# Kernel tuning notes

Hardware: AMD Instinct MI355X
Metric: run time of the kernel (lower is better)

Reference implementation:

```python
import jax, jax.numpy as jnp
import numpy as np


def setup_inputs() -> dict:
    key = jax.random.key(0)
    k1, k2, k3, k4 = jax.random.split(key, 4)
    B, H, W, K = 16, 256, 256, 313
    pred_ab = jax.random.normal(k1, (B, 2, H, W), dtype=jnp.float32)
    # targets in normalized ab range roughly [-1, 1]
    target_ab = jax.random.uniform(k2, (B, 2, H, W), dtype=jnp.float32, minval=-1.0, maxval=1.0)
    # quantized ab gamut centers in denormalized ab space (~[-110, 110])
    ab_centers = jax.random.normal(k3, (K, 2), dtype=jnp.float32) * 60.0
    class_weights = jax.random.uniform(k4, (K,), dtype=jnp.float32, minval=0.1, maxval=5.0)
    return {"pred_ab": pred_ab, "target_ab": target_ab,
            "ab_centers": ab_centers, "class_weights": class_weights}


def reference(pred_ab, target_ab, ab_centers, class_weights):
    B, _, H, W = target_ab.shape
    # per-pixel L2 over the 2 ab channels -> [B, H, W]
    l2_loss = jnp.sum((pred_ab - target_ab) ** 2, axis=1)
    # rebalancing: nearest quantized ab bin per pixel
    target_denorm = target_ab * 128.0
    ab_flat = jnp.transpose(target_denorm, (0, 2, 3, 1)).reshape(-1, 2)  # [N, 2]
    # pairwise squared distances [N, K]
    diff = ab_flat[:, None, :] - ab_centers[None, :, :]
    distances = jnp.sum(diff ** 2, axis=2)
    nearest_bins = jnp.argmin(distances, axis=1)  # [N]
    pixel_weights = class_weights[nearest_bins].reshape(B, H, W)
    return jnp.mean(l2_loss * pixel_weights)
```

## Files before the change

kernel.cpp:

```cpp
#include <hip/hip_runtime.h>
#include <math.h>

#define HW     (256 * 256)
#define NPIX   (16 * HW)
#define KMAX   320
#define BLOCK  256
#define PPT    4
#define MAIN_GRID (NPIX / (BLOCK * PPT))

__global__ __launch_bounds__(BLOCK)
void build_lut_kernel(const float* __restrict__ centers,
                      const float* __restrict__ weights,
                      int K, int G, int lgG, float cellsz,
                      float* __restrict__ lut,
                      float* __restrict__ out)
{
    if (blockIdx.x == 0 && threadIdx.x == 0) out[0] = 0.0f;

    __shared__ float4 cc[KMAX];
    for (int k = threadIdx.x; k < K; k += BLOCK) {
        float cx = centers[2 * k];
        float cy = centers[2 * k + 1];
        cc[k] = make_float4(cx, cy, fmaf(cx, cx, cy * cy), weights[k]);
    }
    __syncthreads();

    int cell = blockIdx.x * BLOCK + threadIdx.x;
    if (cell >= (G << lgG)) return;
    int ix = cell & (G - 1);
    int iy = cell >> lgG;
    float x = fmaf((float)ix + 0.5f, cellsz, -128.0f);
    float y = fmaf((float)iy + 0.5f, cellsz, -128.0f);
    float ax = -2.0f * x, ay = -2.0f * y;
    float best = INFINITY, bw = 0.0f;
    for (int k = 0; k < K; k++) {
        float4 c = cc[k];
        float s = fmaf(c.x, ax, fmaf(c.y, ay, c.z));
        if (s < best) { best = s; bw = c.w; }
    }
    lut[cell] = bw;
}

__global__ __launch_bounds__(BLOCK)
void main_kernel(const float* __restrict__ pred,
                 const float* __restrict__ targ,
                 const float* __restrict__ lut,
                 int G, int lgG, float G2,
                 float* __restrict__ out)
{
    int n = blockIdx.x * (BLOCK * PPT) + (threadIdx.x << 2);
    int b = n >> 16;
    int p = n & (HW - 1);
    const float* pb = pred + (size_t)b * 2 * HW;
    const float* tb = targ + (size_t)b * 2 * HW;
    float4 T0 = *(const float4*)(tb + p);
    float4 T1 = *(const float4*)(tb + HW + p);
    float4 P0 = *(const float4*)(pb + p);
    float4 P1 = *(const float4*)(pb + HW + p);

    float t0[4] = {T0.x, T0.y, T0.z, T0.w};
    float t1[4] = {T1.x, T1.y, T1.z, T1.w};
    float p0[4] = {P0.x, P0.y, P0.z, P0.w};
    float p1[4] = {P1.x, P1.y, P1.z, P1.w};

    int gmax = G - 1;
    float w[4];
    #pragma unroll
    for (int i = 0; i < 4; i++) {
        float fx = fmaf(t0[i], G2, G2);
        float fy = fmaf(t1[i], G2, G2);
        int ix = (int)fx; ix = ix < 0 ? 0 : (ix > gmax ? gmax : ix);
        int iy = (int)fy; iy = iy < 0 ? 0 : (iy > gmax ? gmax : iy);
        w[i] = lut[(iy << lgG) + ix];
    }

    float sum = 0.0f;
    #pragma unroll
    for (int i = 0; i < 4; i++) {
        float d0 = p0[i] - t0[i];
        float d1 = p1[i] - t1[i];
        sum = fmaf(fmaf(d0, d0, d1 * d1), w[i], sum);
    }

    #pragma unroll
    for (int off = 32; off; off >>= 1) sum += __shfl_down(sum, off, 64);
    __shared__ float wsum[BLOCK / 64];
    int lane = threadIdx.x & 63, wid = threadIdx.x >> 6;
    if (lane == 0) wsum[wid] = sum;
    __syncthreads();

    if (threadIdx.x == 0) {
        float bsum = wsum[0] + wsum[1] + wsum[2] + wsum[3];
        atomicAdd(out, bsum * (1.0f / (float)NPIX));
    }
}

extern "C" void kernel_launch(void* const* d_in, const int* in_sizes, int n_in,
                              void* d_out, int out_size, void* d_ws, size_t ws_size,
                              hipStream_t stream)
{
    const float* pred    = (const float*)d_in[0];
    const float* targ    = (const float*)d_in[1];
    const float* centers = (const float*)d_in[2];
    const float* weights = (const float*)d_in[3];
    const int K = in_sizes[3];

    float* lut = (float*)d_ws;
    float* out = (float*)d_out;

    int G, lgG;
    if (ws_size >= 256u * 256u * 4u)      { G = 256; lgG = 8; }
    else if (ws_size >= 128u * 128u * 4u) { G = 128; lgG = 7; }
    else                                  { G = 64;  lgG = 6; }
    float cellsz = 256.0f / (float)G;
    float G2     = (float)G * 0.5f;

    int lut_blocks = (G * G + BLOCK - 1) / BLOCK;
    build_lut_kernel<<<lut_blocks, BLOCK, 0, stream>>>(centers, weights, K, G, lgG,
                                                       cellsz, lut, out);
    main_kernel<<<MAIN_GRID, BLOCK, 0, stream>>>(pred, targ, lut, G, lgG, G2, out);
}
```

Before: 94.54 us.

## Split LUT argmin across warps over center ranges and reduce in shared memory

The LUT build kernel now has each thread evaluate four grid cells, and each of the four wavefronts in a block scans a quarter of the K centers. A shared-memory pass then merges the partial minima, so each center read from LDS is reused across four cells and each wave's serial loop is about a quarter as long. The goal is to cut the latency of the LUT build, which runs before the main kernel. In exchange it adds a block barrier and partial-result traffic through shared memory. Index ties between wavefronts go to the lower index, which matches the earlier strict-less-than scan.

```diff
diff --git a/kernel.cpp b/kernel.cpp
--- a/kernel.cpp
+++ b/kernel.cpp
@@ -17,28 +17,59 @@
 {
     if (blockIdx.x == 0 && threadIdx.x == 0) out[0] = 0.0f;
 
-    __shared__ float4 cc[KMAX];
+    __shared__ float2 cxy[KMAX];
+    __shared__ float  cw[KMAX];
+    __shared__ float2 part[4][BLOCK];
+
     for (int k = threadIdx.x; k < K; k += BLOCK) {
-        float cx = centers[2 * k];
-        float cy = centers[2 * k + 1];
-        cc[k] = make_float4(cx, cy, fmaf(cx, cx, cy * cy), weights[k]);
+        cxy[k] = ((const float2*)centers)[k];
+        cw[k]  = weights[k];
     }
     __syncthreads();
 
-    int cell = blockIdx.x * BLOCK + threadIdx.x;
-    if (cell >= (G << lgG)) return;
-    int ix = cell & (G - 1);
-    int iy = cell >> lgG;
-    float x = fmaf((float)ix + 0.5f, cellsz, -128.0f);
-    float y = fmaf((float)iy + 0.5f, cellsz, -128.0f);
-    float ax = -2.0f * x, ay = -2.0f * y;
-    float best = INFINITY, bw = 0.0f;
-    for (int k = 0; k < K; k++) {
-        float4 c = cc[k];
-        float s = fmaf(c.x, ax, fmaf(c.y, ay, c.z));
-        if (s < best) { best = s; bw = c.w; }
+    int lane = threadIdx.x & 63, wid = threadIdx.x >> 6;
+    int cell0 = blockIdx.x * BLOCK;
+
+    float ax[4], ay[4];
+    #pragma unroll
+    for (int j = 0; j < 4; j++) {
+        int cell = cell0 + lane + 64 * j;
+        int ix = cell & (G - 1);
+        int iy = cell >> lgG;
+        ax[j] = -2.0f * fmaf((float)ix + 0.5f, cellsz, -128.0f);
+        ay[j] = -2.0f * fmaf((float)iy + 0.5f, cellsz, -128.0f);
     }
-    lut[cell] = bw;
+
+    int kpw = (K + 3) >> 2;
+    int k0 = wid * kpw;
+    int k1 = k0 + kpw; if (k1 > K) k1 = K;
+
+    float bs[4] = {INFINITY, INFINITY, INFINITY, INFINITY};
+    int   bk[4] = {0, 0, 0, 0};
+    #pragma unroll 4
+    for (int k = k0; k < k1; k++) {
+        float2 c = cxy[k];
+        float cz = fmaf(c.x, c.x, c.y * c.y);
+        #pragma unroll
+        for (int j = 0; j < 4; j++) {
+            float s = fmaf(c.x, ax[j], fmaf(c.y, ay[j], cz));
+            if (s < bs[j]) { bs[j] = s; bk[j] = k; }
+        }
+    }
+
+    #pragma unroll
+    for (int j = 0; j < 4; j++)
+        part[wid][lane + 64 * j] = make_float2(bs[j], (float)bk[j]);
+    __syncthreads();
+
+    int t = threadIdx.x;
+    float2 best = part[0][t];
+    #pragma unroll
+    for (int w = 1; w < 4; w++) {
+        float2 p = part[w][t];
+        if (p.x < best.x) best = p;
+    }
+    lut[cell0 + t] = cw[(int)best.y];
 }
 
 __global__ __launch_bounds__(BLOCK)
@@ -115,7 +146,7 @@
     float cellsz = 256.0f / (float)G;
     float G2     = (float)G * 0.5f;
 
-    int lut_blocks = (G * G + BLOCK - 1) / BLOCK;
+    int lut_blocks = (G * G) / BLOCK;
     build_lut_kernel<<<lut_blocks, BLOCK, 0, stream>>>(centers, weights, K, G, lgG,
                                                        cellsz, lut, out);
     main_kernel<<<MAIN_GRID, BLOCK, 0, stream>>>(pred, targ, lut, G, lgG, G2, out);
```

Result: faster. 91.36 us (-3.4%).
